# Kernel optimization log

Hardware: AMD Instinct MI355X
Metric: run time of the kernel (lower is better)

Reference implementation:

```python
import jax, jax.numpy as jnp
import numpy as np

D_MODEL = 512
D_STATE = 64
D_CONV = 4
D_INNER = 1024   # expand=2 * d_model (mamba_ssm default)
DT_RANK = 32     # ceil(d_model/16)
NUM_CLASSES = 8
B, T, P, F = 8, 250, 20, 24   # x: [B, T*P=5000, F=24]
FLAT = T * P * F              # 120000 = fc1 input dim


def _mamba(u, in_proj_w, conv_w, conv_b, x_proj_w, dt_proj_w, dt_proj_b, A_log, D, out_proj_w):
    # u: [b, L, d_model]
    b, L, _ = u.shape
    xz = jnp.einsum('bld,ed->ble', u, in_proj_w)      # [b, L, 2*d_inner]
    x, z = jnp.split(xz, 2, axis=-1)                  # each [b, L, d_inner]
    # depthwise causal conv1d, kernel width D_CONV, truncated to L
    x_pad = jnp.pad(x, ((0, 0), (D_CONV - 1, 0), (0, 0)))
    x = sum(x_pad[:, k:k + L, :] * conv_w[:, k] for k in range(D_CONV)) + conv_b
    x = jax.nn.silu(x)
    x_dbl = jnp.einsum('bld,ed->ble', x, x_proj_w)    # [b, L, dt_rank + 2*d_state]
    dt, Bm, Cm = jnp.split(x_dbl, [DT_RANK, DT_RANK + D_STATE], axis=-1)
    dt = jax.nn.softplus(jnp.einsum('blr,dr->bld', dt, dt_proj_w) + dt_proj_b)  # [b, L, d_inner]
    A = -jnp.exp(A_log)                               # [d_inner, d_state]

    def step(h, inp):
        dt_t, B_t, C_t, u_t = inp                     # [b,d_in], [b,d_st], [b,d_st], [b,d_in]
        dA = jnp.exp(dt_t[:, :, None] * A)            # [b, d_in, d_st]
        dBu = dt_t[:, :, None] * B_t[:, None, :] * u_t[:, :, None]
        h = h * dA + dBu
        y = jnp.einsum('bds,bs->bd', h, C_t)
        return h, y

    xs = (jnp.swapaxes(dt, 0, 1), jnp.swapaxes(Bm, 0, 1), jnp.swapaxes(Cm, 0, 1), jnp.swapaxes(x, 0, 1))
    h0 = jnp.zeros((b, D_INNER, D_STATE), dtype=u.dtype)
    _, ys = jax.lax.scan(step, h0, xs)                # ys: [L, b, d_inner]
    y = jnp.swapaxes(ys, 0, 1) + x * D
    y = y * jax.nn.silu(z)
    return jnp.einsum('bld,ed->ble', y, out_proj_w)   # [b, L, d_model]


def setup_inputs() -> dict:
    key = jax.random.key(0)
    ks = jax.random.split(key, 16)
    n = lambda k, shape, s=0.02: jax.random.normal(k, shape, jnp.float32) * s
    return {
        'x': jax.random.normal(ks[0], (B, T * P, F), jnp.float32),
        'in_proj_w': n(ks[1], (2 * D_INNER, D_MODEL)),
        'conv_w': n(ks[2], (D_INNER, D_CONV), 0.1),
        'conv_b': jnp.zeros((D_INNER,), jnp.float32),
        'x_proj_w': n(ks[3], (DT_RANK + 2 * D_STATE, D_INNER)),
        'dt_proj_w': n(ks[4], (D_INNER, DT_RANK), 0.1),
        'dt_proj_b': jnp.full((D_INNER,), -4.6, jnp.float32),  # softplus -> dt ~ 0.01
        'A_log': jnp.log(jnp.broadcast_to(jnp.arange(1, D_STATE + 1, dtype=jnp.float32), (D_INNER, D_STATE))),
        'D': jnp.ones((D_INNER,), jnp.float32),
        'out_proj_w': n(ks[5], (D_MODEL, D_INNER)),
        'fc1_w': n(ks[6], (512, FLAT), 0.003),
        'fc1_b': jnp.zeros((512,), jnp.float32),
        'fc2_w': n(ks[7], (256, 512)),
        'fc2_b': jnp.zeros((256,), jnp.float32),
        'fc3_w': n(ks[8], (64, 256)),
        'fc3_b': jnp.zeros((64,), jnp.float32),
        'fc4_w': n(ks[9], (NUM_CLASSES, 64)),
        'fc4_b': jnp.zeros((NUM_CLASSES,), jnp.float32),
    }


def reference(x, in_proj_w, conv_w, conv_b, x_proj_w, dt_proj_w, dt_proj_b, A_log, D, out_proj_w,
              fc1_w, fc1_b, fc2_w, fc2_b, fc3_w, fc3_b, fc4_w, fc4_b):
    b = x.shape[0]
    u = x.reshape(b, T, P * F)                                   # [b,250,480]
    u = jnp.pad(u, ((0, 0), (0, 0), (0, D_MODEL - P * F)))       # pad 480 -> 512
    y = _mamba(u, in_proj_w, conv_w, conv_b, x_proj_w, dt_proj_w, dt_proj_b, A_log, D, out_proj_w)
    y = jax.nn.selu(y)                                           # AlphaDropout: identity in eval
    y = y[..., :P * F].reshape(b, T * P, F)                      # [b,5000,24]
    y = jnp.swapaxes(y, 1, 2).reshape(b, -1)                     # [b, 24*5000]
    y = y @ fc1_w.T + fc1_b
    y = y @ fc2_w.T + fc2_b
    y = y @ fc3_w.T + fc3_b
    return y @ fc4_w.T + fc4_b
```

## Files before the change

### kernel.cpp

```cpp
#include <hip/hip_runtime.h>
#include <math.h>

#define T_ 250
#define BL 2000
#define KIN 480
#define NFLAT 120000

__device__ __forceinline__ float sigmoidf_(float x){ return 1.0f/(1.0f+expf(-x)); }
__device__ __forceinline__ float siluf_(float x){ return x*sigmoidf_(x); }
__device__ __forceinline__ float softplusf_(float x){ return (x > 20.0f) ? x : log1pf(expf(x)); }
__device__ __forceinline__ float seluf_(float x){
  const float sc = 1.0507009873554804934193349852946f;
  const float al = 1.6732632423543772848170429916717f;
  return x > 0.0f ? sc*x : sc*al*expm1f(x);
}

template<int CTRL>
__device__ __forceinline__ float dpp_add(float x) {
  int t = __builtin_amdgcn_update_dpp(0, __builtin_bit_cast(int, x), CTRL, 0xF, 0xF, true);
  return x + __builtin_bit_cast(float, t);
}

template<int BM, int BN, int BK, int TM, int TN>
__global__ __launch_bounds__(256, 2) void gemm_nt(
    const float* __restrict__ A, const float* __restrict__ W,
    float* __restrict__ C, const float* __restrict__ bias,
    int M, int N, int K, int lda, int ldb, int ldc, int epi)
{
  static_assert(BK == 32, "BK must be 32");
  __shared__ __align__(16) float As[BK][BM + 4];
  __shared__ __align__(16) float Bs[BK][BN + 4];
  constexpr int TNX = BN / TN;
  constexpr int TMX = BM / TM;
  static_assert(TNX * TMX == 256, "256 threads required");
  constexpr int AF4 = BM * BK / 1024;
  constexpr int BF4 = BN * BK / 1024;

  const int tid = threadIdx.x;
  const int tx = tid % TNX;
  const int ty = tid / TNX;
  const int m0 = blockIdx.y * BM;
  const int n0 = blockIdx.x * BN;
  const int kchunk = K / (int)gridDim.z;
  const int k_begin = blockIdx.z * kchunk;
  const int k_end = k_begin + kchunk;

  float4 pa[AF4], pb[BF4];

  auto fetch = [&](int k0) {
#pragma unroll
    for (int i = 0; i < AF4; ++i) {
      int fi = tid + 256 * i;
      int r = fi >> 3;
      int kc = (fi & 7) * 4;
      int m = m0 + r;
      pa[i] = (m < M) ? *(const float4*)(A + (size_t)m * lda + k0 + kc)
                      : make_float4(0.f, 0.f, 0.f, 0.f);
    }
#pragma unroll
    for (int i = 0; i < BF4; ++i) {
      int fi = tid + 256 * i;
      int r = fi >> 3;
      int kc = (fi & 7) * 4;
      int n = n0 + r;
      pb[i] = (n < N) ? *(const float4*)(W + (size_t)n * ldb + k0 + kc)
                      : make_float4(0.f, 0.f, 0.f, 0.f);
    }
  };

  fetch(k_begin);

  float acc[TM][TN];
#pragma unroll
  for (int i = 0; i < TM; ++i)
#pragma unroll
    for (int j = 0; j < TN; ++j) acc[i][j] = 0.0f;

  for (int k0 = k_begin; k0 < k_end; k0 += BK) {
#pragma unroll
    for (int i = 0; i < AF4; ++i) {
      int fi = tid + 256 * i;
      int r = fi >> 3;
      int kc = (fi & 7) * 4;
      As[kc + 0][r] = pa[i].x; As[kc + 1][r] = pa[i].y;
      As[kc + 2][r] = pa[i].z; As[kc + 3][r] = pa[i].w;
    }
#pragma unroll
    for (int i = 0; i < BF4; ++i) {
      int fi = tid + 256 * i;
      int r = fi >> 3;
      int kc = (fi & 7) * 4;
      Bs[kc + 0][r] = pb[i].x; Bs[kc + 1][r] = pb[i].y;
      Bs[kc + 2][r] = pb[i].z; Bs[kc + 3][r] = pb[i].w;
    }
    __syncthreads();
    if (k0 + BK < k_end) fetch(k0 + BK);
#pragma unroll
    for (int kk = 0; kk < BK; ++kk) {
      float a[TM], bb[TN];
      if constexpr ((TM & 3) == 0) {
#pragma unroll
        for (int t = 0; t < TM / 4; ++t) {
          float4 v = *(const float4*)&As[kk][ty * TM + t * 4];
          a[t*4+0] = v.x; a[t*4+1] = v.y; a[t*4+2] = v.z; a[t*4+3] = v.w;
        }
      } else {
#pragma unroll
        for (int i = 0; i < TM; ++i) a[i] = As[kk][ty * TM + i];
      }
      if constexpr ((TN & 3) == 0) {
#pragma unroll
        for (int t = 0; t < TN / 4; ++t) {
          float4 v = *(const float4*)&Bs[kk][tx * TN + t * 4];
          bb[t*4+0] = v.x; bb[t*4+1] = v.y; bb[t*4+2] = v.z; bb[t*4+3] = v.w;
        }
      } else {
#pragma unroll
        for (int j = 0; j < TN; ++j) bb[j] = Bs[kk][tx * TN + j];
      }
#pragma unroll
      for (int i = 0; i < TM; ++i)
#pragma unroll
        for (int j = 0; j < TN; ++j) acc[i][j] = fmaf(a[i], bb[j], acc[i][j]);
    }
    __syncthreads();
  }

  if (epi == 4) {
#pragma unroll
    for (int i = 0; i < TM; ++i) {
      int m = m0 + ty * TM + i;
      if (m >= M) continue;
      int b = m / 250;
      int tt = m - b * 250;
#pragma unroll
      for (int j = 0; j < TN; ++j) {
        int n = n0 + tx * TN + j;
        if (n >= N) continue;
        int p = n / 24;
        int f = n - p * 24;
        C[(size_t)b * NFLAT + (size_t)f * 5000 + tt * 20 + p] = seluf_(acc[i][j]);
      }
    }
    return;
  }

#pragma unroll
  for (int i = 0; i < TM; ++i) {
    int m = m0 + ty * TM + i;
    if (m >= M) continue;
    if constexpr ((TN & 3) == 0) {
#pragma unroll
      for (int j0 = 0; j0 < TN; j0 += 4) {
        int n = n0 + tx * TN + j0;
        float v[4];
#pragma unroll
        for (int t = 0; t < 4; ++t) {
          float xv = acc[i][j0 + t];
          if (epi == 1) xv = softplusf_(xv + bias[n + t]);
          else if (epi == 2) xv = seluf_(xv);
          v[t] = xv;
        }
        if (epi == 3) {
#pragma unroll
          for (int t = 0; t < 4; ++t)
            if (n + t < N) atomicAdd(&C[(size_t)m * ldc + n + t], v[t]);
        } else if (n + 3 < N) {
          *(float4*)&C[(size_t)m * ldc + n] = make_float4(v[0], v[1], v[2], v[3]);
        } else {
#pragma unroll
          for (int t = 0; t < 4; ++t)
            if (n + t < N) C[(size_t)m * ldc + n + t] = v[t];
        }
      }
    } else {
#pragma unroll
      for (int j = 0; j < TN; ++j) {
        int n = n0 + tx * TN + j;
        if (n >= N) continue;
        float v = acc[i][j];
        if (epi == 1) v = softplusf_(v + bias[n]);
        else if (epi == 2) v = seluf_(v);
        if (epi == 3) atomicAdd(&C[(size_t)m * ldc + n], v);
        else C[(size_t)m * ldc + n] = v;
      }
    }
  }
}

__global__ __launch_bounds__(256) void conv_silu(
    float* __restrict__ xz, const float* __restrict__ cw,
    const float* __restrict__ cb, float* __restrict__ xc)
{
  int id = blockIdx.x * 256 + threadIdx.x;
  if (id >= BL * 1024) return;
  int bl = id >> 10;
  int d = id & 1023;
  int l = bl % T_;
  float4 w4 = *(const float4*)(cw + d * 4);
  float s = cb[d];
  if (l >= 3) s = fmaf(xz[(size_t)(bl - 3) * 2048 + d], w4.x, s);
  if (l >= 2) s = fmaf(xz[(size_t)(bl - 2) * 2048 + d], w4.y, s);
  if (l >= 1) s = fmaf(xz[(size_t)(bl - 1) * 2048 + d], w4.z, s);
  s = fmaf(xz[(size_t)bl * 2048 + d], w4.w, s);
  xc[id] = siluf_(s);
  float z = xz[(size_t)bl * 2048 + 1024 + d];
  xz[(size_t)bl * 2048 + 1024 + d] = siluf_(z);
}

__global__ __launch_bounds__(256) void scan_kernel(
    const float* __restrict__ dtb, const float* __restrict__ xc,
    const float* __restrict__ xdbl, float* __restrict__ xz,
    const float* __restrict__ A_log, const float* __restrict__ Dp)
{
  int tid = threadIdx.x;
  int wv = tid >> 6, lane = tid & 63;
  int c = lane >> 5;
  int u = lane & 31;
  int w = blockIdx.x * 4 + wv;
  int b = w >> 9;
  int d = ((w & 511) << 1) + c;
  const float LOG2E = 1.4426950408889634f;
  float2 al = *(const float2*)(A_log + (size_t)d * 64 + u * 2);
  float am0 = -expf(al.x) * LOG2E;
  float am1 = -expf(al.y) * LOG2E;
  float Dv = Dp[d];
  float h0 = 0.f, h1 = 0.f;
  const float* dtp = dtb + (size_t)b * 256000 + d;
  const float* xp  = xc  + (size_t)b * 256000 + d;
  const float* zp  = xz  + (size_t)b * 512000 + 1024 + d;
  float*       yp  = xz  + (size_t)b * 512000 + d;
  const float* bp  = xdbl + (size_t)b * 40000 + 32 + u * 2;
  const float* cp  = bp + 64;

  float dt_f[4], xv_f[4], sz_f[4];
  float2 B_f[4], C_f[4];
#pragma unroll
  for (int i = 0; i < 4; ++i) {
    dt_f[i] = dtp[(size_t)i * 1024];
    xv_f[i] = xp[(size_t)i * 1024];
    sz_f[i] = zp[(size_t)i * 2048];
    B_f[i] = *(const float2*)(bp + (size_t)i * 160);
    C_f[i] = *(const float2*)(cp + (size_t)i * 160);
  }
  const bool outlane = (u == 16);

#pragma unroll 4
  for (int l = 0; l < 252; ++l) {
    int slot = l & 3;
    float dt = dt_f[slot], xv = xv_f[slot], sz = sz_f[slot];
    float2 Bv = B_f[slot], Cv = C_f[slot];
    dt_f[slot] = dtp[(size_t)(l + 4) * 1024];
    xv_f[slot] = xp[(size_t)(l + 4) * 1024];
    sz_f[slot] = zp[(size_t)(l + 4) * 2048];
    B_f[slot]  = *(const float2*)(bp + (size_t)(l + 4) * 160);
    C_f[slot]  = *(const float2*)(cp + (size_t)(l + 4) * 160);

    float dtx = dt * xv;
    h0 = fmaf(h0, exp2f(dt * am0), dtx * Bv.x);
    h1 = fmaf(h1, exp2f(dt * am1), dtx * Bv.y);
    float p = fmaf(h1, Cv.y, h0 * Cv.x);
    p = dpp_add<0xB1>(p);
    p = dpp_add<0x4E>(p);
    p = dpp_add<0x124>(p);
    p = dpp_add<0x128>(p);
    p = dpp_add<0x142>(p);
    if (outlane && l < T_) yp[(size_t)l * 2048] = fmaf(xv, Dv, p) * sz;
  }
}

__global__ __launch_bounds__(256) void fc1_kernel(
    const float* __restrict__ yfl, const float* __restrict__ W,
    float* __restrict__ r1)
{
  int blk = blockIdx.x;
  int ks = blk % 24;
  int cg = blk / 24;
  int wv = threadIdx.x >> 6;
  int lane = threadIdx.x & 63;
  int c0 = cg * 16 + wv * 4;
  const float* W0 = W + (size_t)c0 * NFLAT;
  float acc[4][8];
#pragma unroll
  for (int cc = 0; cc < 4; ++cc)
#pragma unroll
    for (int b = 0; b < 8; ++b) acc[cc][b] = 0.0f;

  int kbase = ks * 5000;
  int kend = kbase + 5000;
  for (int k = kbase + lane * 4; k + 4 <= kend; k += 256) {
    float4 w0 = *(const float4*)(W0 + k);
    float4 w1 = *(const float4*)(W0 + NFLAT + k);
    float4 w2 = *(const float4*)(W0 + 2 * (size_t)NFLAT + k);
    float4 w3 = *(const float4*)(W0 + 3 * (size_t)NFLAT + k);
#pragma unroll
    for (int b = 0; b < 8; ++b) {
      float4 y = *(const float4*)(yfl + (size_t)b * NFLAT + k);
      acc[0][b] = fmaf(w0.x, y.x, fmaf(w0.y, y.y, fmaf(w0.z, y.z, fmaf(w0.w, y.w, acc[0][b]))));
      acc[1][b] = fmaf(w1.x, y.x, fmaf(w1.y, y.y, fmaf(w1.z, y.z, fmaf(w1.w, y.w, acc[1][b]))));
      acc[2][b] = fmaf(w2.x, y.x, fmaf(w2.y, y.y, fmaf(w2.z, y.z, fmaf(w2.w, y.w, acc[2][b]))));
      acc[3][b] = fmaf(w3.x, y.x, fmaf(w3.y, y.y, fmaf(w3.z, y.z, fmaf(w3.w, y.w, acc[3][b]))));
    }
  }
#pragma unroll
  for (int cc = 0; cc < 4; ++cc)
#pragma unroll
    for (int b = 0; b < 8; ++b) {
      float s = acc[cc][b];
      s += __shfl_xor(s, 1);
      s += __shfl_xor(s, 2);
      s += __shfl_xor(s, 4);
      s += __shfl_xor(s, 8);
      s += __shfl_xor(s, 16);
      s += __shfl_xor(s, 32);
      if (lane == 0) atomicAdd(&r1[b * 512 + c0 + cc], s);
    }
}

__global__ __launch_bounds__(256) void fc2_kernel(
    const float* __restrict__ r1, const float* __restrict__ b1,
    const float* __restrict__ W2, const float* __restrict__ b2,
    float* __restrict__ r2)
{
  int wid = blockIdx.x * 4 + (threadIdx.x >> 6);
  int lane = threadIdx.x & 63;
  int b = wid >> 8;
  int j = wid & 255;
  int off = lane * 8;
  float4 ya = *(const float4*)(r1 + b * 512 + off);
  float4 yb = *(const float4*)(r1 + b * 512 + off + 4);
  float4 ba = *(const float4*)(b1 + off);
  float4 bbv = *(const float4*)(b1 + off + 4);
  float4 wa = *(const float4*)(W2 + (size_t)j * 512 + off);
  float4 wb = *(const float4*)(W2 + (size_t)j * 512 + off + 4);
  float p = (ya.x + ba.x) * wa.x + (ya.y + ba.y) * wa.y +
            (ya.z + ba.z) * wa.z + (ya.w + ba.w) * wa.w +
            (yb.x + bbv.x) * wb.x + (yb.y + bbv.y) * wb.y +
            (yb.z + bbv.z) * wb.z + (yb.w + bbv.w) * wb.w;
  p += __shfl_xor(p, 1);
  p += __shfl_xor(p, 2);
  p += __shfl_xor(p, 4);
  p += __shfl_xor(p, 8);
  p += __shfl_xor(p, 16);
  p += __shfl_xor(p, 32);
  if (lane == 0) r2[b * 256 + j] = p + b2[j];
}

__global__ __launch_bounds__(256) void fc34_kernel(
    const float* __restrict__ r2, const float* __restrict__ W3,
    const float* __restrict__ b3, const float* __restrict__ W4,
    const float* __restrict__ b4, float* __restrict__ out)
{
  __shared__ float a3[512];
  int tid = threadIdx.x;
  for (int o = tid; o < 512; o += 256) {
    int b = o >> 6, j = o & 63;
    float s = b3[j];
    const float* rr = r2 + b * 256;
    const float* wr = W3 + j * 256;
    for (int c = 0; c < 256; c += 4) {
      float4 rv = *(const float4*)(rr + c);
      float4 wv = *(const float4*)(wr + c);
      s = fmaf(rv.x, wv.x, fmaf(rv.y, wv.y, fmaf(rv.z, wv.z, fmaf(rv.w, wv.w, s))));
    }
    a3[o] = s;
  }
  __syncthreads();
  if (tid < 64) {
    int b = tid >> 3, j = tid & 7;
    float s = b4[j];
    const float* ar = a3 + b * 64;
    const float* wr = W4 + j * 64;
    for (int c = 0; c < 64; ++c) s = fmaf(ar[c], wr[c], s);
    out[b * 8 + j] = s;
  }
}

extern "C" void kernel_launch(void* const* d_in, const int* in_sizes, int n_in,
                              void* d_out, int out_size, void* d_ws, size_t ws_size,
                              hipStream_t stream) {
  const float* x      = (const float*)d_in[0];
  const float* w_in   = (const float*)d_in[1];
  const float* conv_w = (const float*)d_in[2];
  const float* conv_b = (const float*)d_in[3];
  const float* w_xp   = (const float*)d_in[4];
  const float* w_dt   = (const float*)d_in[5];
  const float* b_dt   = (const float*)d_in[6];
  const float* A_log  = (const float*)d_in[7];
  const float* Dp     = (const float*)d_in[8];
  const float* w_out  = (const float*)d_in[9];
  const float* w1 = (const float*)d_in[10];
  const float* b1 = (const float*)d_in[11];
  const float* w2 = (const float*)d_in[12];
  const float* b2 = (const float*)d_in[13];
  const float* w3 = (const float*)d_in[14];
  const float* b3 = (const float*)d_in[15];
  const float* w4 = (const float*)d_in[16];
  const float* b4 = (const float*)d_in[17];
  float* out = (float*)d_out;

  float* ws   = (float*)d_ws;
  float* xz   = ws;
  float* xc   = xz + 4096000;
  float* dtb  = xc + 2048000;
  float* ym   = dtb + 2048000;
  float* yfl  = ym + 960000;
  float* xdbl = yfl + 960000;
  float* r1   = xdbl + 320000;
  float* r2   = r1 + 4096;
  (void)ym;

  hipMemsetAsync(xdbl, 0, (320000 + 4096) * sizeof(float), stream);

  gemm_nt<64, 128, 32, 4, 8><<<dim3(2048 / 128, (BL + 63) / 64, 1), 256, 0, stream>>>(
      x, w_in, xz, nullptr, BL, 2048, KIN, KIN, 512, 2048, 0);

  conv_silu<<<(BL * 1024) / 256, 256, 0, stream>>>(xz, conv_w, conv_b, xc);

  gemm_nt<32, 64, 32, 1, 8><<<dim3(3, (BL + 31) / 32, 2), 256, 0, stream>>>(
      xc, w_xp, xdbl, nullptr, BL, 160, 1024, 1024, 1024, 160, 3);

  gemm_nt<32, 64, 32, 1, 8><<<dim3(1024 / 64, (BL + 31) / 32, 1), 256, 0, stream>>>(
      xdbl, w_dt, dtb, b_dt, BL, 1024, 32, 160, 32, 1024, 1);

  scan_kernel<<<1024, 256, 0, stream>>>(dtb, xc, xdbl, xz, A_log, Dp);

  gemm_nt<64, 64, 32, 4, 4><<<dim3((KIN + 63) / 64, (BL + 63) / 64, 1), 256, 0, stream>>>(
      xz, w_out, yfl, nullptr, BL, KIN, 1024, 2048, 1024, KIN, 4);

  fc1_kernel<<<768, 256, 0, stream>>>(yfl, w1, r1);

  fc2_kernel<<<512, 256, 0, stream>>>(r1, b1, w2, b2, r2);

  fc34_kernel<<<1, 256, 0, stream>>>(r2, w3, b3, w4, b4, out);
}
```

Baseline: 686.5 us.

## Add register-prefetched 128x128 GEMM, split-K out_proj with separate transpose-SELU

Replaces the in_proj GEMM with a new 128x128-tile kernel that prefetches the next K-slice into registers while computing on shared memory. The x_proj GEMM gets larger tiles and a higher split-K factor. The out_proj GEMM now uses split-K with atomics into a zeroed buffer, and its fused scatter-SELU epilogue moves into a separate transpose_selu kernel. The intent is more parallelism and better reuse in the GEMMs, paid for with extra atomics, a larger memset and one more kernel launch and pass over memory.

```diff
diff --git a/kernel.cpp b/kernel.cpp
--- a/kernel.cpp
+++ b/kernel.cpp
@@ -126,25 +126,6 @@
     __syncthreads();
   }
 
-  if (epi == 4) {
-#pragma unroll
-    for (int i = 0; i < TM; ++i) {
-      int m = m0 + ty * TM + i;
-      if (m >= M) continue;
-      int b = m / 250;
-      int tt = m - b * 250;
-#pragma unroll
-      for (int j = 0; j < TN; ++j) {
-        int n = n0 + tx * TN + j;
-        if (n >= N) continue;
-        int p = n / 24;
-        int f = n - p * 24;
-        C[(size_t)b * NFLAT + (size_t)f * 5000 + tt * 20 + p] = seluf_(acc[i][j]);
-      }
-    }
-    return;
-  }
-
 #pragma unroll
   for (int i = 0; i < TM; ++i) {
     int m = m0 + ty * TM + i;
@@ -183,6 +164,96 @@
         else if (epi == 2) v = seluf_(v);
         if (epi == 3) atomicAdd(&C[(size_t)m * ldc + n], v);
         else C[(size_t)m * ldc + n] = v;
+      }
+    }
+  }
+}
+
+__global__ __launch_bounds__(256, 1) void gemm_nt_big(
+    const float* __restrict__ A, const float* __restrict__ W,
+    float* __restrict__ C, int M, int N, int K, int lda, int ldb, int ldc)
+{
+  __shared__ __align__(16) float As[32][132];
+  __shared__ __align__(16) float Bs[32][132];
+  const int tid = threadIdx.x;
+  const int tx = tid & 15;
+  const int ty = tid >> 4;
+  const int rg = tid & 31;
+  const int kg = tid >> 5;
+  const int m0 = blockIdx.y * 128;
+  const int n0 = blockIdx.x * 128;
+
+  float pa[4][4], pb[4][4];
+
+  auto fetch = [&](int k0) {
+#pragma unroll
+    for (int i = 0; i < 4; ++i) {
+      int m = m0 + rg * 4 + i;
+      float4 v = make_float4(0.f, 0.f, 0.f, 0.f);
+      if (m < M) v = *(const float4*)(A + (size_t)m * lda + k0 + kg * 4);
+      pa[i][0] = v.x; pa[i][1] = v.y; pa[i][2] = v.z; pa[i][3] = v.w;
+    }
+#pragma unroll
+    for (int i = 0; i < 4; ++i) {
+      int n = n0 + rg * 4 + i;
+      float4 v = make_float4(0.f, 0.f, 0.f, 0.f);
+      if (n < N) v = *(const float4*)(W + (size_t)n * ldb + k0 + kg * 4);
+      pb[i][0] = v.x; pb[i][1] = v.y; pb[i][2] = v.z; pb[i][3] = v.w;
+    }
+  };
+
+  fetch(0);
+
+  float acc[8][8];
+#pragma unroll
+  for (int i = 0; i < 8; ++i)
+#pragma unroll
+    for (int j = 0; j < 8; ++j) acc[i][j] = 0.0f;
+
+  for (int k0 = 0; k0 < K; k0 += 32) {
+#pragma unroll
+    for (int j = 0; j < 4; ++j)
+      *(float4*)&As[kg * 4 + j][rg * 4] =
+          make_float4(pa[0][j], pa[1][j], pa[2][j], pa[3][j]);
+#pragma unroll
+    for (int j = 0; j < 4; ++j)
+      *(float4*)&Bs[kg * 4 + j][rg * 4] =
+          make_float4(pb[0][j], pb[1][j], pb[2][j], pb[3][j]);
+    __syncthreads();
+    if (k0 + 32 < K) fetch(k0 + 32);
+#pragma unroll
+    for (int kk = 0; kk < 32; ++kk) {
+      float a[8], bb[8];
+      float4 v0 = *(const float4*)&As[kk][ty * 8];
+      float4 v1 = *(const float4*)&As[kk][ty * 8 + 4];
+      a[0]=v0.x; a[1]=v0.y; a[2]=v0.z; a[3]=v0.w;
+      a[4]=v1.x; a[5]=v1.y; a[6]=v1.z; a[7]=v1.w;
+      float4 w0 = *(const float4*)&Bs[kk][tx * 8];
+      float4 w1 = *(const float4*)&Bs[kk][tx * 8 + 4];
+      bb[0]=w0.x; bb[1]=w0.y; bb[2]=w0.z; bb[3]=w0.w;
+      bb[4]=w1.x; bb[5]=w1.y; bb[6]=w1.z; bb[7]=w1.w;
+#pragma unroll
+      for (int i = 0; i < 8; ++i)
+#pragma unroll
+        for (int j = 0; j < 8; ++j) acc[i][j] = fmaf(a[i], bb[j], acc[i][j]);
+    }
+    __syncthreads();
+  }
+
+#pragma unroll
+  for (int i = 0; i < 8; ++i) {
+    int m = m0 + ty * 8 + i;
+    if (m >= M) continue;
+#pragma unroll
+    for (int j0 = 0; j0 < 8; j0 += 4) {
+      int n = n0 + tx * 8 + j0;
+      if (n + 3 < N) {
+        *(float4*)&C[(size_t)m * ldc + n] =
+            make_float4(acc[i][j0], acc[i][j0+1], acc[i][j0+2], acc[i][j0+3]);
+      } else {
+#pragma unroll
+        for (int t = 0; t < 4; ++t)
+          if (n + t < N) C[(size_t)m * ldc + n + t] = acc[i][j0 + t];
       }
     }
   }
@@ -267,6 +338,20 @@
     p = dpp_add<0x142>(p);
     if (outlane && l < T_) yp[(size_t)l * 2048] = fmaf(xv, Dv, p) * sz;
   }
+}
+
+__global__ __launch_bounds__(256) void transpose_selu(
+    const float* __restrict__ ym, float* __restrict__ yfl)
+{
+  int id = blockIdx.x * 256 + threadIdx.x;
+  if (id >= 8 * NFLAT) return;
+  int b = id / NFLAT;
+  int r = id % NFLAT;
+  int f = r / 5000;
+  int qq = r % 5000;
+  int tt = qq / 20;
+  int p = qq % 20;
+  yfl[id] = seluf_(ym[(size_t)(b * T_ + tt) * KIN + p * 24 + f]);
 }
 
 __global__ __launch_bounds__(256) void fc1_kernel(
@@ -403,21 +488,20 @@
   float* xz   = ws;
   float* xc   = xz + 4096000;
   float* dtb  = xc + 2048000;
-  float* ym   = dtb + 2048000;
-  float* yfl  = ym + 960000;
+  float* yfl  = dtb + 2048000;
   float* xdbl = yfl + 960000;
   float* r1   = xdbl + 320000;
   float* r2   = r1 + 4096;
-  (void)ym;
-
-  hipMemsetAsync(xdbl, 0, (320000 + 4096) * sizeof(float), stream);
-
-  gemm_nt<64, 128, 32, 4, 8><<<dim3(2048 / 128, (BL + 63) / 64, 1), 256, 0, stream>>>(
-      x, w_in, xz, nullptr, BL, 2048, KIN, KIN, 512, 2048, 0);
+  float* ym   = r2 + 2048;
+
+  hipMemsetAsync(xdbl, 0, (320000 + 4096 + 2048 + 960000) * sizeof(float), stream);
+
+  gemm_nt_big<<<dim3(2048 / 128, (BL + 127) / 128, 1), 256, 0, stream>>>(
+      x, w_in, xz, BL, 2048, KIN, KIN, 512, 2048);
 
   conv_silu<<<(BL * 1024) / 256, 256, 0, stream>>>(xz, conv_w, conv_b, xc);
 
-  gemm_nt<32, 64, 32, 1, 8><<<dim3(3, (BL + 31) / 32, 2), 256, 0, stream>>>(
+  gemm_nt<64, 64, 32, 4, 4><<<dim3(3, (BL + 63) / 64, 4), 256, 0, stream>>>(
       xc, w_xp, xdbl, nullptr, BL, 160, 1024, 1024, 1024, 160, 3);
 
   gemm_nt<32, 64, 32, 1, 8><<<dim3(1024 / 64, (BL + 31) / 32, 1), 256, 0, stream>>>(
@@ -425,8 +509,10 @@
 
   scan_kernel<<<1024, 256, 0, stream>>>(dtb, xc, xdbl, xz, A_log, Dp);
 
-  gemm_nt<64, 64, 32, 4, 4><<<dim3((KIN + 63) / 64, (BL + 63) / 64, 1), 256, 0, stream>>>(
-      xz, w_out, yfl, nullptr, BL, KIN, 1024, 2048, 1024, KIN, 4);
+  gemm_nt<64, 64, 32, 4, 4><<<dim3((KIN + 63) / 64, (BL + 63) / 64, 4), 256, 0, stream>>>(
+      xz, w_out, ym, nullptr, BL, KIN, 1024, 2048, 1024, KIN, 3);
+
+  transpose_selu<<<(8 * NFLAT) / 256, 256, 0, stream>>>(ym, yfl);
 
   fc1_kernel<<<768, 256, 0, stream>>>(yfl, w1, r1);
 
```

Result: slower. 708.1 us (+3.1%).

## Use bf16 MFMA for in_proj GEMM and vectorize conv_silu

Applied to the files above, without the earlier changes.

Replaces the fp32 SIMT tiled GEMM for the input projection with a 128x128-tile kernel that rounds x and weights to bf16 in shared memory and issues 16x16x32 bf16 MFMA instructions, with register prefetch of the next K slice. The conv+SiLU kernel now handles four channels per thread using float4 loads and stores. The aim is to cut the in_proj compute time and the elementwise memory traffic, at the cost of bf16 rounding error in the projection output.

```diff
diff --git a/kernel.cpp b/kernel.cpp
--- a/kernel.cpp
+++ b/kernel.cpp
@@ -5,6 +5,9 @@
 #define BL 2000
 #define KIN 480
 #define NFLAT 120000
+
+typedef __attribute__((ext_vector_type(8))) short short8;
+typedef __attribute__((ext_vector_type(4))) float f32x4;
 
 __device__ __forceinline__ float sigmoidf_(float x){ return 1.0f/(1.0f+expf(-x)); }
 __device__ __forceinline__ float siluf_(float x){ return x*sigmoidf_(x); }
@@ -14,11 +17,101 @@
   const float al = 1.6732632423543772848170429916717f;
   return x > 0.0f ? sc*x : sc*al*expm1f(x);
 }
+__device__ __forceinline__ unsigned f2bf(float f){
+  unsigned u = __builtin_bit_cast(unsigned, f);
+  return (u + 0x7FFFu + ((u >> 16) & 1u)) >> 16;
+}
 
 template<int CTRL>
 __device__ __forceinline__ float dpp_add(float x) {
   int t = __builtin_amdgcn_update_dpp(0, __builtin_bit_cast(int, x), CTRL, 0xF, 0xF, true);
   return x + __builtin_bit_cast(float, t);
+}
+
+__global__ __launch_bounds__(256) void inproj_mfma(
+    const float* __restrict__ x, const float* __restrict__ w,
+    float* __restrict__ C)
+{
+  __shared__ __align__(16) unsigned short As[128 * 40];
+  __shared__ __align__(16) unsigned short Bs[128 * 40];
+  const int tid = threadIdx.x;
+  const int m0 = blockIdx.y * 128;
+  const int n0 = blockIdx.x * 128;
+  const int wid = tid >> 6, lane = tid & 63;
+  const int wr = wid >> 1, wc = wid & 1;
+  const int sr = tid >> 1;
+  const int sk = (tid & 1) * 16;
+  const int fr = lane & 15, fg = lane >> 4;
+
+  float4 pa[4], pb[4];
+  auto fetch = [&](int k0) {
+    int m = m0 + sr;
+    if (m < BL) {
+      const float* xp = x + (size_t)m * KIN + k0 + sk;
+      pa[0] = *(const float4*)(xp);
+      pa[1] = *(const float4*)(xp + 4);
+      pa[2] = *(const float4*)(xp + 8);
+      pa[3] = *(const float4*)(xp + 12);
+    } else {
+      pa[0] = pa[1] = pa[2] = pa[3] = make_float4(0.f, 0.f, 0.f, 0.f);
+    }
+    const float* wp = w + (size_t)(n0 + sr) * 512 + k0 + sk;
+    pb[0] = *(const float4*)(wp);
+    pb[1] = *(const float4*)(wp + 4);
+    pb[2] = *(const float4*)(wp + 8);
+    pb[3] = *(const float4*)(wp + 12);
+  };
+  auto pack2 = [](float a, float b) {
+    return f2bf(a) | (f2bf(b) << 16);
+  };
+  auto stash = [&](unsigned short* S, float4* p) {
+    uint4 lo = make_uint4(pack2(p[0].x, p[0].y), pack2(p[0].z, p[0].w),
+                          pack2(p[1].x, p[1].y), pack2(p[1].z, p[1].w));
+    uint4 hi = make_uint4(pack2(p[2].x, p[2].y), pack2(p[2].z, p[2].w),
+                          pack2(p[3].x, p[3].y), pack2(p[3].z, p[3].w));
+    *(uint4*)&S[sr * 40 + sk] = lo;
+    *(uint4*)&S[sr * 40 + sk + 8] = hi;
+  };
+
+  f32x4 acc[4][4];
+#pragma unroll
+  for (int i = 0; i < 4; ++i)
+#pragma unroll
+    for (int j = 0; j < 4; ++j) acc[i][j] = (f32x4)(0.0f);
+
+  fetch(0);
+  for (int k0 = 0; k0 < KIN; k0 += 32) {
+    stash(As, pa);
+    stash(Bs, pb);
+    __syncthreads();
+    if (k0 + 32 < KIN) fetch(k0 + 32);
+    short8 av[4], bv[4];
+#pragma unroll
+    for (int fi = 0; fi < 4; ++fi)
+      av[fi] = *(const short8*)&As[(wr * 64 + fi * 16 + fr) * 40 + fg * 8];
+#pragma unroll
+    for (int fj = 0; fj < 4; ++fj)
+      bv[fj] = *(const short8*)&Bs[(wc * 64 + fj * 16 + fr) * 40 + fg * 8];
+#pragma unroll
+    for (int fi = 0; fi < 4; ++fi)
+#pragma unroll
+      for (int fj = 0; fj < 4; ++fj)
+        acc[fi][fj] = __builtin_amdgcn_mfma_f32_16x16x32_bf16(
+            av[fi], bv[fj], acc[fi][fj], 0, 0, 0);
+    __syncthreads();
+  }
+
+#pragma unroll
+  for (int fi = 0; fi < 4; ++fi) {
+    int row = m0 + wr * 64 + fi * 16 + fg * 4;
+#pragma unroll
+    for (int fj = 0; fj < 4; ++fj) {
+      int col = n0 + wc * 64 + fj * 16 + fr;
+#pragma unroll
+      for (int r = 0; r < 4; ++r)
+        if (row + r < BL) C[(size_t)(row + r) * 2048 + col] = acc[fi][fj][r];
+    }
+  }
 }
 
 template<int BM, int BN, int BK, int TM, int TN>
@@ -193,19 +286,29 @@
     const float* __restrict__ cb, float* __restrict__ xc)
 {
   int id = blockIdx.x * 256 + threadIdx.x;
-  if (id >= BL * 1024) return;
-  int bl = id >> 10;
-  int d = id & 1023;
+  if (id >= BL * 256) return;
+  int bl = id >> 8;
+  int d4 = (id & 255) * 4;
   int l = bl % T_;
-  float4 w4 = *(const float4*)(cw + d * 4);
-  float s = cb[d];
-  if (l >= 3) s = fmaf(xz[(size_t)(bl - 3) * 2048 + d], w4.x, s);
-  if (l >= 2) s = fmaf(xz[(size_t)(bl - 2) * 2048 + d], w4.y, s);
-  if (l >= 1) s = fmaf(xz[(size_t)(bl - 1) * 2048 + d], w4.z, s);
-  s = fmaf(xz[(size_t)bl * 2048 + d], w4.w, s);
-  xc[id] = siluf_(s);
-  float z = xz[(size_t)bl * 2048 + 1024 + d];
-  xz[(size_t)bl * 2048 + 1024 + d] = siluf_(z);
+  float* base = xz + (size_t)bl * 2048 + d4;
+  float4 x0 = *(const float4*)(base);
+  float4 x1 = (l >= 1) ? *(const float4*)(base - 2048) : make_float4(0.f,0.f,0.f,0.f);
+  float4 x2 = (l >= 2) ? *(const float4*)(base - 4096) : make_float4(0.f,0.f,0.f,0.f);
+  float4 x3 = (l >= 3) ? *(const float4*)(base - 6144) : make_float4(0.f,0.f,0.f,0.f);
+  float4 w0 = *(const float4*)(cw + (size_t)d4 * 4);
+  float4 w1 = *(const float4*)(cw + (size_t)d4 * 4 + 4);
+  float4 w2 = *(const float4*)(cw + (size_t)d4 * 4 + 8);
+  float4 w3 = *(const float4*)(cw + (size_t)d4 * 4 + 12);
+  float4 cbv = *(const float4*)(cb + d4);
+  float4 o;
+  o.x = siluf_(fmaf(x3.x, w0.x, fmaf(x2.x, w0.y, fmaf(x1.x, w0.z, fmaf(x0.x, w0.w, cbv.x)))));
+  o.y = siluf_(fmaf(x3.y, w1.x, fmaf(x2.y, w1.y, fmaf(x1.y, w1.z, fmaf(x0.y, w1.w, cbv.y)))));
+  o.z = siluf_(fmaf(x3.z, w2.x, fmaf(x2.z, w2.y, fmaf(x1.z, w2.z, fmaf(x0.z, w2.w, cbv.z)))));
+  o.w = siluf_(fmaf(x3.w, w3.x, fmaf(x2.w, w3.y, fmaf(x1.w, w3.z, fmaf(x0.w, w3.w, cbv.w)))));
+  *(float4*)(xc + (size_t)bl * 1024 + d4) = o;
+  float4 zv = *(const float4*)(base + 1024);
+  zv.x = siluf_(zv.x); zv.y = siluf_(zv.y); zv.z = siluf_(zv.z); zv.w = siluf_(zv.w);
+  *(float4*)(base + 1024) = zv;
 }
 
 __global__ __launch_bounds__(256) void scan_kernel(
@@ -412,10 +515,9 @@
 
   hipMemsetAsync(xdbl, 0, (320000 + 4096) * sizeof(float), stream);
 
-  gemm_nt<64, 128, 32, 4, 8><<<dim3(2048 / 128, (BL + 63) / 64, 1), 256, 0, stream>>>(
-      x, w_in, xz, nullptr, BL, 2048, KIN, KIN, 512, 2048, 0);
-
-  conv_silu<<<(BL * 1024) / 256, 256, 0, stream>>>(xz, conv_w, conv_b, xc);
+  inproj_mfma<<<dim3(2048 / 128, 16, 1), 256, 0, stream>>>(x, w_in, xz);
+
+  conv_silu<<<(BL * 256) / 256, 256, 0, stream>>>(xz, conv_w, conv_b, xc);
 
   gemm_nt<32, 64, 32, 1, 8><<<dim3(3, (BL + 31) / 32, 2), 256, 0, stream>>>(
       xc, w_xp, xdbl, nullptr, BL, 160, 1024, 1024, 1024, 160, 3);
```

Measured after the change: 645.9 us. -5.9%, faster.
